# Kernel tuning notes

Measured on AMD Instinct MI355X. Metric: run time of the kernel, lower is better.

## Reference

```python
import jax, jax.numpy as jnp
import numpy as np

NUM_CAMS, BS, NUM_QUERY, MAX_LEN, EMBED_DIMS, NPTS = 6, 1, 40000, 10000, 256, 4


def setup_inputs() -> dict:
    key = jax.random.key(0)
    kq, kr, km = jax.random.split(key, 3)
    query = jax.random.normal(kq, (BS, NUM_QUERY, EMBED_DIMS), dtype=jnp.float32)
    reference_points_cam = jax.random.normal(
        kr, (NUM_CAMS, BS, NUM_QUERY, NPTS, 2), dtype=jnp.float32)
    bev_mask = jax.random.randint(km, (NUM_CAMS, BS, NUM_QUERY, NPTS), 0, 2).astype(jnp.int32)
    return {"query": query, "reference_points_cam": reference_points_cam, "bev_mask": bev_mask}


def reference(query, reference_points_cam, bev_mask):
    # valid[c, q]: query q is seen by camera c (any of the NPTS mask bits set); bs == 1
    valid = (bev_mask > 0).any(-1)            # (cams, bs, Q) bool
    valid0 = valid[:, 0]                      # (cams, Q)

    # Stable stream compaction: valid indices first, in ascending query order.
    order = jnp.argsort(~valid0, axis=-1, stable=True)      # (cams, Q)
    indexes = order[:, :MAX_LEN].astype(jnp.int32)          # (cams, max_len)
    indexes_len = jnp.minimum(valid0.sum(-1), MAX_LEN).astype(jnp.int32)  # (cams,)

    # Padded gather/rebatch; zero out slots beyond each camera's valid count.
    pos_ok = jnp.arange(MAX_LEN)[None, :] < indexes_len[:, None]          # (cams, max_len)
    queries_rebatch = query[0][indexes]                                   # (cams, max_len, E)
    queries_rebatch = jnp.where(pos_ok[:, :, None], queries_rebatch, 0.0)

    ref0 = reference_points_cam[:, 0]                                     # (cams, Q, NPTS, 2)
    reference_points_rebatch = jax.vmap(lambda r, i: r[i])(ref0, indexes) # (cams, max_len, NPTS, 2)
    reference_points_rebatch = jnp.where(
        pos_ok[:, :, None, None], reference_points_rebatch, 0.0)

    # count_norm: 1 / (number of cameras that see each query, clamped to >= 1)
    count = valid.astype(jnp.float32).sum(0)                 # (bs, Q)
    count_norm = (1.0 / jnp.maximum(count, 1.0))[..., None]  # (bs, Q, 1)

    return (indexes,
            indexes_len,
            queries_rebatch.reshape(BS * NUM_CAMS, MAX_LEN, EMBED_DIMS),
            reference_points_rebatch.reshape(BS * NUM_CAMS, MAX_LEN, NPTS, 2),
            count_norm)
```

## Files before the change

### kernel.cpp

```cpp
#include <hip/hip_runtime.h>
#include <hip/hip_bf16.h>

#define NUM_CAMS 6
#define NQ       40000
#define MAX_LEN  10000
#define ED       256

typedef float f32x2 __attribute__((ext_vector_type(2)));

#define OFF_IDX  0
#define OFF_LEN  (NUM_CAMS * MAX_LEN)
#define OFF_Q    (OFF_LEN + NUM_CAMS)
#define OFF_REF  (OFF_Q + NUM_CAMS * MAX_LEN * ED)
#define OFF_CNT  (OFF_REF + NUM_CAMS * MAX_LEN * 8)

#define WS_LEN 0

#define GATHER_BLOCKS (NUM_CAMS * MAX_LEN / 4)
#define CNT_BLOCKS    ((NQ + 255) / 256)

__global__ __launch_bounds__(1024) void kScan(const int* __restrict__ bev,
                                              float* __restrict__ out,
                                              int* __restrict__ ws) {
    const int cam  = blockIdx.x;
    const int tid  = threadIdx.x;
    const int lane = tid & 63;
    const int wave = tid >> 6;
    __shared__ int wsum[16];
    const int* bevc = bev + (size_t)cam * NQ * 4;

    int running = 0;
    int4 cur = *reinterpret_cast<const int4*>(bevc + (size_t)tid * 4);
    for (int base = 0; base < NQ; base += 1024) {
        const int q  = base + tid;
        const int qn = q + 1024;
        int4 nxt = make_int4(0, 0, 0, 0);
        if (qn < NQ) nxt = *reinterpret_cast<const int4*>(bevc + (size_t)qn * 4);

        const bool v = (q < NQ) && ((cur.x > 0) | (cur.y > 0) | (cur.z > 0) | (cur.w > 0));
        const unsigned long long bal = __ballot(v);
        if (lane == 0) wsum[wave] = __popcll(bal);
        __syncthreads();
        int wOff = 0, chunkTot = 0;
        #pragma unroll
        for (int w = 0; w < 16; ++w) {
            const int s = wsum[w];
            if (w < wave) wOff += s;
            chunkTot += s;
        }
        if (v) {
            const int pos = running + wOff + __popcll(bal & ((1ull << lane) - 1ull));
            if (pos < MAX_LEN) out[OFF_IDX + cam * MAX_LEN + pos] = (float)q;
        }
        running += chunkTot;
        __syncthreads();
        if (running >= MAX_LEN) break;
        cur = nxt;
    }
    const int total = running;
    const int len   = total < MAX_LEN ? total : MAX_LEN;

    if (total < MAX_LEN) {
        int runInv = 0;
        for (int base = 0; base < NQ; base += 1024) {
            const int q = base + tid;
            bool v = false;
            if (q < NQ) {
                const int4 m = *reinterpret_cast<const int4*>(bevc + (size_t)q * 4);
                v = (m.x > 0) | (m.y > 0) | (m.z > 0) | (m.w > 0);
            }
            const bool inv = (q < NQ) && !v;
            const unsigned long long bal = __ballot(inv);
            if (lane == 0) wsum[wave] = __popcll(bal);
            __syncthreads();
            int wOff = 0, chunkTot = 0;
            #pragma unroll
            for (int w = 0; w < 16; ++w) {
                const int s = wsum[w];
                if (w < wave) wOff += s;
                chunkTot += s;
            }
            if (inv) {
                const int pos = total + runInv + wOff + __popcll(bal & ((1ull << lane) - 1ull));
                if (pos < MAX_LEN) out[OFF_IDX + cam * MAX_LEN + pos] = (float)q;
            }
            runInv += chunkTot;
            __syncthreads();
            if (total + runInv >= MAX_LEN) break;
        }
    }
    if (tid == 0) {
        ws[WS_LEN + cam] = len;
        out[OFF_LEN + cam] = (float)len;
    }
}

__global__ void kGather(const float* __restrict__ query, const float* __restrict__ refp,
                        float* __restrict__ out, const int* __restrict__ ws,
                        const int* __restrict__ bev) {
    const int blk = blockIdx.x;
    const int tid = threadIdx.x;
    if (blk >= GATHER_BLOCKS) {
        const int q = (blk - GATHER_BLOCKS) * 256 + tid;
        if (q < NQ) {
            int cnt = 0;
            #pragma unroll
            for (int cam = 0; cam < NUM_CAMS; ++cam) {
                const int4 m = *reinterpret_cast<const int4*>(bev + ((size_t)cam * NQ + q) * 4);
                cnt += ((m.x > 0) | (m.y > 0) | (m.z > 0) | (m.w > 0)) ? 1 : 0;
            }
            out[OFF_CNT + q] = 1.0f / fmaxf((float)cnt, 1.0f);
        }
        return;
    }
    const int rowId = blk * 4 + (tid >> 6);
    const int lane  = tid & 63;
    const int cam   = rowId / MAX_LEN;
    const int j     = rowId - cam * MAX_LEN;
    const int len   = ws[WS_LEN + cam];

    f32x2 a = (f32x2)(0.f), b = (f32x2)(0.f), r0 = (f32x2)(0.f), r1 = (f32x2)(0.f);
    if (j < len) {
        const int idx = (int)out[OFF_IDX + cam * MAX_LEN + j];
        const float4 vq = *reinterpret_cast<const float4*>(query + (size_t)idx * ED + lane * 4);
        a.x = vq.x; a.y = vq.y;
        b.x = vq.z; b.y = vq.w;
        if (lane < 2) {
            const float4 r = *reinterpret_cast<const float4*>(refp + ((size_t)cam * NQ + idx) * 8 + lane * 4);
            r0.x = r.x; r0.y = r.y;
            r1.x = r.z; r1.y = r.w;
        }
    }
    f32x2* o2 = reinterpret_cast<f32x2*>(out + OFF_Q + (size_t)rowId * ED + lane * 4);
    __builtin_nontemporal_store(a, o2);
    __builtin_nontemporal_store(b, o2 + 1);
    if (lane < 2) {
        f32x2* r2 = reinterpret_cast<f32x2*>(out + OFF_REF + (size_t)rowId * 8 + lane * 4);
        r2[0] = r0;
        r2[1] = r1;
    }
}

extern "C" void kernel_launch(void* const* d_in, const int* in_sizes, int n_in,
                              void* d_out, int out_size, void* d_ws, size_t ws_size,
                              hipStream_t stream) {
    const float* query = (const float*)d_in[0];
    const float* refp  = (const float*)d_in[1];
    const int*   bev   = (const int*)d_in[2];
    float* out = (float*)d_out;
    int*   ws  = (int*)d_ws;

    kScan<<<NUM_CAMS, 1024, 0, stream>>>(bev, out, ws);
    kGather<<<GATHER_BLOCKS + CNT_BLOCKS, 256, 0, stream>>>(query, refp, out, ws, bev);
}
```

Before: 36.79 us.

## Scatter gather by query with per-camera positions to reuse query reads

The scan now records, for each camera and query, the output slot of each valid query, plus the query at which it stopped. A new query-major gather kernel reads each query row once and scatters it to every camera slot that needs it, instead of reading it once per camera. A separate small kernel zero-fills the padded tail rows. This adds a 960KB position workspace write, an extra launch, and a 6-block tail kernel that may serialize. It falls back to the old path if the workspace is too small.

```diff
diff --git a/kernel.cpp b/kernel.cpp
--- a/kernel.cpp
+++ b/kernel.cpp
@@ -15,13 +15,17 @@
 #define OFF_CNT  (OFF_REF + NUM_CAMS * MAX_LEN * 8)
 
 #define WS_LEN 0
-
+#define WS_CUT 6
+#define WS_POS 12
+#define WS_NEED_BYTES ((WS_POS + NUM_CAMS * NQ) * 4)
+
+#define QBLOCKS   (NQ / 4)
+#define CNT_BLOCKS ((NQ + 255) / 256)
 #define GATHER_BLOCKS (NUM_CAMS * MAX_LEN / 4)
-#define CNT_BLOCKS    ((NQ + 255) / 256)
 
 __global__ __launch_bounds__(1024) void kScan(const int* __restrict__ bev,
                                               float* __restrict__ out,
-                                              int* __restrict__ ws) {
+                                              int* __restrict__ ws, int usePos) {
     const int cam  = blockIdx.x;
     const int tid  = threadIdx.x;
     const int lane = tid & 63;
@@ -30,6 +34,7 @@
     const int* bevc = bev + (size_t)cam * NQ * 4;
 
     int running = 0;
+    int qEnd = NQ;
     int4 cur = *reinterpret_cast<const int4*>(bevc + (size_t)tid * 4);
     for (int base = 0; base < NQ; base += 1024) {
         const int q  = base + tid;
@@ -48,13 +53,12 @@
             if (w < wave) wOff += s;
             chunkTot += s;
         }
-        if (v) {
-            const int pos = running + wOff + __popcll(bal & ((1ull << lane) - 1ull));
-            if (pos < MAX_LEN) out[OFF_IDX + cam * MAX_LEN + pos] = (float)q;
-        }
+        const int pos = running + wOff + __popcll(bal & ((1ull << lane) - 1ull));
+        if (v && pos < MAX_LEN) out[OFF_IDX + cam * MAX_LEN + pos] = (float)q;
+        if (usePos && q < NQ) ws[WS_POS + cam * NQ + q] = (v && pos < MAX_LEN) ? pos : -1;
         running += chunkTot;
         __syncthreads();
-        if (running >= MAX_LEN) break;
+        if (running >= MAX_LEN) { qEnd = base + 1024; break; }
         cur = nxt;
     }
     const int total = running;
@@ -91,7 +95,75 @@
     }
     if (tid == 0) {
         ws[WS_LEN + cam] = len;
+        ws[WS_CUT + cam] = qEnd;
         out[OFF_LEN + cam] = (float)len;
+    }
+}
+
+__global__ __launch_bounds__(1024) void kTail(float* __restrict__ out,
+                                              const int* __restrict__ ws) {
+    const int cam   = blockIdx.x;
+    const int len   = ws[WS_LEN + cam];
+    const int group = threadIdx.x >> 6;
+    const int lane  = threadIdx.x & 63;
+    const f32x2 z = (f32x2)(0.f);
+    for (int j = len + group; j < MAX_LEN; j += 16) {
+        f32x2* o2 = reinterpret_cast<f32x2*>(out + OFF_Q + ((size_t)cam * MAX_LEN + j) * ED + lane * 4);
+        o2[0] = z; o2[1] = z;
+        if (lane < 4)
+            *reinterpret_cast<f32x2*>(out + OFF_REF + ((size_t)cam * MAX_LEN + j) * 8 + lane * 2) = z;
+    }
+}
+
+__global__ void kGatherQ(const float* __restrict__ query, const float* __restrict__ refp,
+                         float* __restrict__ out, const int* __restrict__ ws,
+                         const int* __restrict__ bev) {
+    const int blk = blockIdx.x;
+    const int tid = threadIdx.x;
+    if (blk >= QBLOCKS) {
+        const int q = (blk - QBLOCKS) * 256 + tid;
+        if (q < NQ) {
+            int cnt = 0;
+            #pragma unroll
+            for (int cam = 0; cam < NUM_CAMS; ++cam) {
+                const int4 m = *reinterpret_cast<const int4*>(bev + ((size_t)cam * NQ + q) * 4);
+                cnt += ((m.x > 0) | (m.y > 0) | (m.z > 0) | (m.w > 0)) ? 1 : 0;
+            }
+            out[OFF_CNT + q] = 1.0f / fmaxf((float)cnt, 1.0f);
+        }
+        return;
+    }
+    const int group = tid >> 6;
+    const int lane  = tid & 63;
+    const int q     = blk * 4 + group;
+
+    int pos[NUM_CAMS];
+    bool any = false;
+    #pragma unroll
+    for (int cam = 0; cam < NUM_CAMS; ++cam) {
+        int p = -1;
+        if (q < ws[WS_CUT + cam]) p = ws[WS_POS + cam * NQ + q];
+        pos[cam] = p;
+        any |= (p >= 0);
+    }
+    if (!any) return;
+
+    const float4 vq = *reinterpret_cast<const float4*>(query + (size_t)q * ED + lane * 4);
+    f32x2 a; a.x = vq.x; a.y = vq.y;
+    f32x2 b; b.x = vq.z; b.y = vq.w;
+
+    #pragma unroll
+    for (int cam = 0; cam < NUM_CAMS; ++cam) {
+        const int p = pos[cam];
+        if (p >= 0) {
+            f32x2* o2 = reinterpret_cast<f32x2*>(out + OFF_Q + ((size_t)cam * MAX_LEN + p) * ED + lane * 4);
+            __builtin_nontemporal_store(a, o2);
+            __builtin_nontemporal_store(b, o2 + 1);
+            if (lane < 4) {
+                const f32x2 r = *reinterpret_cast<const f32x2*>(refp + ((size_t)cam * NQ + q) * 8 + lane * 2);
+                *reinterpret_cast<f32x2*>(out + OFF_REF + ((size_t)cam * MAX_LEN + p) * 8 + lane * 2) = r;
+            }
+        }
     }
 }
 
@@ -149,7 +221,13 @@
     const int*   bev   = (const int*)d_in[2];
     float* out = (float*)d_out;
     int*   ws  = (int*)d_ws;
-
-    kScan<<<NUM_CAMS, 1024, 0, stream>>>(bev, out, ws);
-    kGather<<<GATHER_BLOCKS + CNT_BLOCKS, 256, 0, stream>>>(query, refp, out, ws, bev);
-}
+    const int usePos = (ws_size >= (size_t)WS_NEED_BYTES) ? 1 : 0;
+
+    kScan<<<NUM_CAMS, 1024, 0, stream>>>(bev, out, ws, usePos);
+    if (usePos) {
+        kTail<<<NUM_CAMS, 1024, 0, stream>>>(out, ws);
+        kGatherQ<<<QBLOCKS + CNT_BLOCKS, 256, 0, stream>>>(query, refp, out, ws, bev);
+    } else {
+        kGather<<<GATHER_BLOCKS + CNT_BLOCKS, 256, 0, stream>>>(query, refp, out, ws, bev);
+    }
+}
```

After: 35.30 us. -4.0%, faster.
